# Optimization experiments

Measured on AMD Instinct MI355X. Metric: run time of the kernel, lower is better.

## Reference

```python
import jax, jax.numpy as jnp
import numpy as np

B, SEQ, DIM = 4, 8192, 512
G = 32              # group_size: number of outer chunks (per source rearrange 'b (g n) d')
QK = 128            # query_key_dim
HD = QK // 4        # head_dim = 32 (used for softmax scale)
HEAD_D = 2 * HD     # per-head feature dim = 64 (h=2 heads over QK)
HID = DIM           # expansion_factor = 1.0
EPS = 1e-5


def _shift_seq(t):
    # F.pad(t, (0,0,1,-1)): prepend one zero row along axis=-2, drop last row
    pad = [(0, 0)] * (t.ndim - 2) + [(1, 0), (0, 0)]
    return jnp.pad(t, pad)[..., :-1, :]


def setup_inputs() -> dict:
    key = jax.random.key(0)
    ks = jax.random.split(key, 8)
    s = 0.02
    return {
        "x": jax.random.normal(ks[0], (B, SEQ, DIM), jnp.float32),
        "ln_g": jnp.ones((DIM,), jnp.float32),
        "ln_b": jnp.zeros((DIM,), jnp.float32),
        "w_qk": jax.random.normal(ks[1], (DIM, QK), jnp.float32) * s,
        "g4": jax.random.normal(ks[2], (4, QK), jnp.float32) * s,   # qk_offset_scale.gamma
        "b4": jnp.zeros((4, QK), jnp.float32),                       # qk_offset_scale.beta
        "g2": jax.random.normal(ks[3], (2, QK), jnp.float32) * s,   # shift_one_offset_scale.gamma
        "b2": jnp.zeros((2, QK), jnp.float32),
        "w_hidden": jax.random.normal(ks[4], (DIM, 2 * HID), jnp.float32) * s,
        "w_gate": jax.random.normal(ks[5], (DIM, HID), jnp.float32) * s,
        "w_out": jax.random.normal(ks[6], (5 * HID, DIM), jnp.float32) * s,
    }


def reference(x, ln_g, ln_b, w_qk, g4, b4, g2, b2, w_hidden, w_gate, w_out):
    b, seq, dim = x.shape
    n = seq // G  # tokens per chunk; seq chosen as multiple of G so padding = 0

    # LayerNorm
    mu = jnp.mean(x, axis=-1, keepdims=True)
    var = jnp.var(x, axis=-1, keepdims=True)
    xs = (x - mu) * jax.lax.rsqrt(var + EPS) * ln_g + ln_b

    # token shift of first half of channels (shift_tokens=True)
    half = dim // 2
    xs = jnp.concatenate([_shift_seq(xs[..., :half]), xs[..., half:]], axis=-1)

    qk = xs @ w_qk                                  # [b, seq, QK]
    qk_g = qk.reshape(b, G, n, QK)                  # 'b (g n) d -> b g n d', g outer
    qk_mean = qk_g.mean(axis=2)                     # [b, G, QK]

    # OffsetScale(heads=4) on per-chunk mean -> q_offset, k_offset, q_scale, k_scale
    offs = qk_mean[:, :, None, :] * g4 + b4         # [b, G, 4, QK]
    q_off, k_off, q_sc, k_sc = (offs[:, :, i, :] for i in range(4))

    q = qk_g * q_sc[:, :, None, :] + q_off[:, :, None, :]   # [b, G, n, QK]
    k = qk_g * k_sc[:, :, None, :] + k_off[:, :, None, :]

    # shift-by-one variants within each chunk, re-scaled + shift-one offsets
    q_s_off = qk_mean * g2[0] + b2[0]               # [b, G, QK]
    k_s_off = qk_mean * g2[1] + b2[1]
    qs = _shift_seq(q) * q_sc[:, :, None, :] + q_s_off[:, :, None, :]
    ks_ = _shift_seq(k) * k_sc[:, :, None, :] + k_s_off[:, :, None, :]

    def heads(t):  # [b,G,n,QK] -> [b,G,2,n,HEAD_D]
        return t.reshape(b, G, n, 2, HEAD_D).transpose(0, 1, 3, 2, 4)

    q_all = jnp.concatenate([heads(q), heads(qs)], axis=2)   # [b,G,4,n,64]
    k_all = jnp.concatenate([heads(k), heads(ks_)], axis=2)

    hg = xs @ w_hidden                              # [b, seq, 2*HID]
    hidden, gate = hg[..., :HID], hg[..., HID:]
    hidden_g = hidden.reshape(b, G, n, HID)

    sim = jnp.einsum('bghid,bghjd->bghij', q_all, k_all) * (HD ** -0.5)
    neg = -jnp.finfo(sim.dtype).max
    causal = jnp.triu(jnp.ones((n, n), dtype=bool), 1)  # applied unconditionally in source
    sim = jnp.where(causal, neg, sim)
    attn = jax.nn.softmax(sim, axis=-1)             # dropout=0 (eval)

    out = jnp.einsum('bghij,bgje->bghie', attn, hidden_g)   # [b,G,4,n,HID]
    gate_g = gate.reshape(b, G, n, HID)
    out = jax.nn.silu(out) * gate_g[:, :, None, :, :]
    out = out.transpose(0, 1, 3, 2, 4).reshape(b, seq, 4 * HID)  # 'b g h n e -> b (g n) (h e)'

    residual = jnp.concatenate([hidden, out], axis=-1)       # [b, seq, 5*HID]
    out = residual @ w_out                                   # [b, seq, dim]
    out = out * jax.nn.silu(xs @ w_gate)
    return out + xs
```

## Files before the change

kernel.cpp:

```cpp
#include <hip/hip_runtime.h>
#include <hip/hip_bf16.h>
#include <math.h>

#define BB 4
#define SEQ 8192
#define DIM 512
#define GG 32
#define NPG 256
#define QKD 128
#define HIDD 512

typedef unsigned short u16;
typedef unsigned int u32;

using s16x8 = __attribute__((ext_vector_type(8))) short;
using f32x4 = __attribute__((ext_vector_type(4))) float;

__device__ __forceinline__ float bf2f(u16 u) { return __uint_as_float(((u32)u) << 16); }
__device__ __forceinline__ u16 f2bf(float f) {
  u32 b = __float_as_uint(f);
  return (u16)((b + 0x7FFFu + ((b >> 16) & 1u)) >> 16);
}
__device__ __forceinline__ float silu_f(float x) { return x / (1.f + expf(-x)); }
__device__ __forceinline__ float silu_fast(float x) { return x / (1.f + __expf(-x)); }
__device__ __forceinline__ float4 fma4(float4 a, float4 b, float4 c) {
  return make_float4(a.x*b.x+c.x, a.y*b.y+c.y, a.z*b.z+c.z, a.w*b.w+c.w);
}
__device__ __forceinline__ float4 mul4(float4 a, float4 b) {
  return make_float4(a.x*b.x, a.y*b.y, a.z*b.z, a.w*b.w);
}
#define LD4(p, off) (*(const float4*)((p) + (off)))

__device__ __forceinline__ void gl_lds16(const u16* g, u16* l) {
  __builtin_amdgcn_global_load_lds((const __attribute__((address_space(1))) void*)g,
                                   (__attribute__((address_space(3))) void*)l, 16, 0, 0);
}

__device__ __forceinline__ s16x8 aff8(s16x8 v, float4 s0, float4 s1, float4 o0, float4 o1) {
  union U { s16x8 x; u16 u[8]; };
  U in; in.x = v; U r;
  r.u[0] = f2bf(bf2f(in.u[0]) * s0.x + o0.x);
  r.u[1] = f2bf(bf2f(in.u[1]) * s0.y + o0.y);
  r.u[2] = f2bf(bf2f(in.u[2]) * s0.z + o0.z);
  r.u[3] = f2bf(bf2f(in.u[3]) * s0.w + o0.w);
  r.u[4] = f2bf(bf2f(in.u[4]) * s1.x + o1.x);
  r.u[5] = f2bf(bf2f(in.u[5]) * s1.y + o1.y);
  r.u[6] = f2bf(bf2f(in.u[6]) * s1.z + o1.z);
  r.u[7] = f2bf(bf2f(in.u[7]) * s1.w + o1.w);
  return r.x;
}
__device__ __forceinline__ s16x8 pack8(float4 a, float4 b) {
  union { s16x8 v; u16 u[8]; } z;
  z.u[0] = f2bf(a.x); z.u[1] = f2bf(a.y); z.u[2] = f2bf(a.z); z.u[3] = f2bf(a.w);
  z.u[4] = f2bf(b.x); z.u[5] = f2bf(b.y); z.u[6] = f2bf(b.z); z.u[7] = f2bf(b.w);
  return z.v;
}

__global__ __launch_bounds__(256) void k_ln(const float* __restrict__ x,
    const float* __restrict__ lg, const float* __restrict__ lb,
    float* __restrict__ xs, u16* __restrict__ xsb) {
  const int row = blockIdx.x;
  const int s = row & (SEQ - 1);
  const int t = threadIdx.x;
  const float* xr = x + (size_t)row * DIM;
  float v0 = xr[t], v1 = xr[t + 256];
  float sum = v0 + v1, sq = v0 * v0 + v1 * v1;
  #pragma unroll
  for (int o = 32; o; o >>= 1) { sum += __shfl_down(sum, o); sq += __shfl_down(sq, o); }
  __shared__ float sm[8];
  const int w = t >> 6;
  if ((t & 63) == 0) { sm[w] = sum; sm[4 + w] = sq; }
  __syncthreads();
  if (t == 0) {
    float S = sm[0] + sm[1] + sm[2] + sm[3];
    float Q = sm[4] + sm[5] + sm[6] + sm[7];
    float mu = S * (1.f / DIM);
    float var = Q * (1.f / DIM) - mu * mu;
    sm[0] = mu; sm[4] = rsqrtf(var + 1e-5f);
  }
  __syncthreads();
  const float mu = sm[0], rs = sm[4];
  float y0 = (v0 - mu) * rs * lg[t] + lb[t];
  float y1 = (v1 - mu) * rs * lg[t + 256] + lb[t + 256];
  xs[(size_t)row * DIM + t + 256] = y1;
  xsb[(size_t)row * DIM + t + 256] = f2bf(y1);
  if (s + 1 < SEQ) {
    xs[(size_t)(row + 1) * DIM + t] = y0;
    xsb[(size_t)(row + 1) * DIM + t] = f2bf(y0);
  }
  if (s == 0) { xs[(size_t)row * DIM + t] = 0.f; xsb[(size_t)row * DIM + t] = 0; }
}

__global__ __launch_bounds__(256) void k_trw(const float* __restrict__ src, u16* __restrict__ dst,
    int N, int dstLD, int rowOff) {
  __shared__ u16 T[64][66];
  const int t = threadIdx.x;
  const int k0 = blockIdx.x * 64, n0 = blockIdx.y * 64;
  #pragma unroll
  for (int i = 0; i < 16; ++i) {
    int idx = t + 256 * i;
    int r = idx >> 6, c = idx & 63;
    T[c][r] = f2bf(src[(size_t)(k0 + r) * N + n0 + c]);
  }
  __syncthreads();
  #pragma unroll
  for (int i = 0; i < 16; ++i) {
    int idx = t + 256 * i;
    int r = idx >> 6, c = idx & 63;
    dst[(size_t)(rowOff + n0 + r) * dstLD + k0 + c] = T[r][c];
  }
}

__global__ __launch_bounds__(256) void k_trh(const u16* __restrict__ hidt, u16* __restrict__ hidr) {
  __shared__ u16 T[64][66];
  const int t = threadIdx.x;
  const int j0 = blockIdx.x * 64;
  const int e0 = blockIdx.y * 64;
  const int bg = blockIdx.z;
  #pragma unroll
  for (int i = 0; i < 16; ++i) {
    int idx = t + 256 * i; int r = idx >> 6, c = idx & 63;
    T[c][r] = hidt[((size_t)bg * 512 + e0 + r) * 256 + j0 + c];
  }
  __syncthreads();
  #pragma unroll
  for (int i = 0; i < 16; ++i) {
    int idx = t + 256 * i; int r = idx >> 6, c = idx & 63;
    hidr[((size_t)bg * 256 + j0 + r) * 512 + e0 + c] = T[r][c];
  }
}

__global__ __launch_bounds__(256, 3) void k_gemm1m(const u16* __restrict__ xsb,
    const u16* __restrict__ w1t, u16* __restrict__ qk, u16* __restrict__ hidt,
    u16* __restrict__ gate, u16* __restrict__ xg) {
  __shared__ u16 As[128 * 64];
  __shared__ u16 Bs[128 * 64];
  const int t = threadIdx.x;
  const int blk = blockIdx.x;
  const int xcd = blk & 7;
  const int loc = blk >> 3;
  const int m0 = (xcd * 32 + loc / 13) * 128;
  const int n0 = (loc % 13) * 128;
  const int w = t >> 6, l = t & 63, lr = l & 15, lq = l >> 4;
  const int wr = (w >> 1) * 64, wc = (w & 1) * 64;
  const int rI = l >> 3;
  const int c8 = (l & 7) ^ rI;
  const int slotA = lq ^ (lr & 7);
  const int slotB = (4 + lq) ^ (lr & 7);
  f32x4 acc[4][4];
  #pragma unroll
  for (int i = 0; i < 4; ++i)
    #pragma unroll
    for (int j = 0; j < 4; ++j) acc[i][j] = (f32x4){0.f, 0.f, 0.f, 0.f};
  for (int tt = 0; tt < 8; ++tt) {
    const int k0 = tt * 64;
    #pragma unroll
    for (int i = 0; i < 4; ++i) {
      const int br = w * 32 + i * 8;
      gl_lds16(xsb + (size_t)(m0 + br + rI) * 512 + k0 + c8 * 8, &As[br * 64]);
      gl_lds16(w1t + (size_t)(n0 + br + rI) * 512 + k0 + c8 * 8, &Bs[br * 64]);
    }
    __syncthreads();
    #pragma unroll
    for (int kk = 0; kk < 2; ++kk) {
      const int slot = kk ? slotB : slotA;
      s16x8 af[4], bf[4];
      #pragma unroll
      for (int fi = 0; fi < 4; ++fi) af[fi] = *(const s16x8*)&As[(wr + fi * 16 + lr) * 64 + slot * 8];
      #pragma unroll
      for (int fj = 0; fj < 4; ++fj) bf[fj] = *(const s16x8*)&Bs[(wc + fj * 16 + lr) * 64 + slot * 8];
      #pragma unroll
      for (int fi = 0; fi < 4; ++fi)
        #pragma unroll
        for (int fj = 0; fj < 4; ++fj)
          acc[fi][fj] = __builtin_amdgcn_mfma_f32_16x16x32_bf16(af[fi], bf[fj], acc[fi][fj], 0, 0, 0);
    }
    __syncthreads();
  }
  if (n0 == 0) {
    #pragma unroll
    for (int fi = 0; fi < 4; ++fi)
      #pragma unroll
      for (int fj = 0; fj < 4; ++fj) {
        const int n = wc + fj * 16 + lr;
        const int mb = m0 + wr + fi * 16 + lq * 4;
        #pragma unroll
        for (int r = 0; r < 4; ++r)
          qk[(size_t)(mb + r) * QKD + n] = f2bf(acc[fi][fj][r]);
      }
  } else if (n0 < 640) {
    const int bg = m0 >> 8;
    #pragma unroll
    for (int fi = 0; fi < 4; ++fi)
      #pragma unroll
      for (int fj = 0; fj < 4; ++fj) {
        const int e = n0 - 128 + wc + fj * 16 + lr;
        const int j0 = (m0 & 255) + wr + fi * 16 + lq * 4;
        ushort4 pk;
        pk.x = f2bf(acc[fi][fj][0]); pk.y = f2bf(acc[fi][fj][1]);
        pk.z = f2bf(acc[fi][fj][2]); pk.w = f2bf(acc[fi][fj][3]);
        *(ushort4*)(hidt + ((size_t)bg * 512 + e) * 256 + j0) = pk;
      }
  } else if (n0 < 1152) {
    #pragma unroll
    for (int fi = 0; fi < 4; ++fi)
      #pragma unroll
      for (int fj = 0; fj < 4; ++fj) {
        const int n = n0 - 640 + wc + fj * 16 + lr;
        const int mb = m0 + wr + fi * 16 + lq * 4;
        #pragma unroll
        for (int r = 0; r < 4; ++r)
          gate[(size_t)(mb + r) * HIDD + n] = f2bf(acc[fi][fj][r]);
      }
  } else {
    #pragma unroll
    for (int fi = 0; fi < 4; ++fi)
      #pragma unroll
      for (int fj = 0; fj < 4; ++fj) {
        const int n = n0 - 1152 + wc + fj * 16 + lr;
        const int mb = m0 + wr + fi * 16 + lq * 4;
        #pragma unroll
        for (int r = 0; r < 4; ++r)
          xg[(size_t)(mb + r) * HIDD + n] = f2bf(silu_f(acc[fi][fj][r]));
      }
  }
}

__global__ __launch_bounds__(128) void k_qkmean(const u16* __restrict__ qk, float* __restrict__ qm) {
  const int bg = blockIdx.x;
  const int c = threadIdx.x;
  const u16* p = qk + (size_t)bg * NPG * QKD + c;
  float s = 0.f;
  for (int i = 0; i < NPG; ++i) s += bf2f(p[(size_t)i * QKD]);
  qm[(size_t)bg * QKD + c] = s * (1.f / NPG);
}

__global__ __launch_bounds__(256, 4) void k_attn(const u16* __restrict__ qk,
    const float* __restrict__ qm, const float* __restrict__ g4, const float* __restrict__ b4,
    const float* __restrict__ g2, const float* __restrict__ b2,
    const u16* __restrict__ hidt, const u16* __restrict__ gate, u16* __restrict__ out4) {
  __shared__ u16 Vs[64][264];
  const int t = threadIdx.x;
  const int l = t & 63;
  const int h = t >> 6;
  const bool sh = (h >= 2);
  const int blk = blockIdx.x;
  const int xcd = blk & 7;
  const int bb = blk >> 3;
  const int bg = xcd * 16 + (bb >> 4);
  const int iw = 15 - (bb & 15);
  const size_t grpRow = (size_t)bg * NPG;
  const int cbase = (h & 1) << 6;
  const int lr = l & 15, lq = l >> 4;
  const int cA = cbase + 8 * lq;
  const int ntmax = iw, jtmax = iw >> 1;
  const int irow = iw * 16 + lr;
  const float* qmp = qm + bg * QKD;
  float4 qmA = LD4(qmp, cA),      qmB = LD4(qmp, cA + 4);
  float4 qmC = LD4(qmp, cA + 32), qmD = LD4(qmp, cA + 36);
  float4 qscA = fma4(qmA, LD4(g4, 2*QKD+cA),    LD4(b4, 2*QKD+cA));
  float4 qscB = fma4(qmB, LD4(g4, 2*QKD+cA+4),  LD4(b4, 2*QKD+cA+4));
  float4 qscC = fma4(qmC, LD4(g4, 2*QKD+cA+32), LD4(b4, 2*QKD+cA+32));
  float4 qscD = fma4(qmD, LD4(g4, 2*QKD+cA+36), LD4(b4, 2*QKD+cA+36));
  float4 qofA = fma4(qmA, LD4(g4, cA),      LD4(b4, cA));
  float4 qofB = fma4(qmB, LD4(g4, cA+4),    LD4(b4, cA+4));
  float4 qofC = fma4(qmC, LD4(g4, cA+32),   LD4(b4, cA+32));
  float4 qofD = fma4(qmD, LD4(g4, cA+36),   LD4(b4, cA+36));
  float4 kscA = fma4(qmA, LD4(g4, 3*QKD+cA),    LD4(b4, 3*QKD+cA));
  float4 kscB = fma4(qmB, LD4(g4, 3*QKD+cA+4),  LD4(b4, 3*QKD+cA+4));
  float4 kscC = fma4(qmC, LD4(g4, 3*QKD+cA+32), LD4(b4, 3*QKD+cA+32));
  float4 kscD = fma4(qmD, LD4(g4, 3*QKD+cA+36), LD4(b4, 3*QKD+cA+36));
  float4 kofA = fma4(qmA, LD4(g4, QKD+cA),      LD4(b4, QKD+cA));
  float4 kofB = fma4(qmB, LD4(g4, QKD+cA+4),    LD4(b4, QKD+cA+4));
  float4 kofC = fma4(qmC, LD4(g4, QKD+cA+32),   LD4(b4, QKD+cA+32));
  float4 kofD = fma4(qmD, LD4(g4, QKD+cA+36),   LD4(b4, QKD+cA+36));
  s16x8 qz0 = {0,0,0,0,0,0,0,0}, qz1 = qz0, kz0 = qz0, kz1 = qz0;
  if (sh) {
    float4 qsoA = fma4(qmA, LD4(g2, cA),    LD4(b2, cA));
    float4 qsoB = fma4(qmB, LD4(g2, cA+4),  LD4(b2, cA+4));
    float4 qsoC = fma4(qmC, LD4(g2, cA+32), LD4(b2, cA+32));
    float4 qsoD = fma4(qmD, LD4(g2, cA+36), LD4(b2, cA+36));
    float4 ksoA = fma4(qmA, LD4(g2, QKD+cA),    LD4(b2, QKD+cA));
    float4 ksoB = fma4(qmB, LD4(g2, QKD+cA+4),  LD4(b2, QKD+cA+4));
    float4 ksoC = fma4(qmC, LD4(g2, QKD+cA+32), LD4(b2, QKD+cA+32));
    float4 ksoD = fma4(qmD, LD4(g2, QKD+cA+36), LD4(b2, QKD+cA+36));
    qofA = fma4(qofA, qscA, qsoA); qofB = fma4(qofB, qscB, qsoB);
    qofC = fma4(qofC, qscC, qsoC); qofD = fma4(qofD, qscD, qsoD);
    qscA = mul4(qscA, qscA); qscB = mul4(qscB, qscB);
    qscC = mul4(qscC, qscC); qscD = mul4(qscD, qscD);
    kofA = fma4(kofA, kscA, ksoA); kofB = fma4(kofB, kscB, ksoB);
    kofC = fma4(kofC, kscC, ksoC); kofD = fma4(kofD, kscD, ksoD);
    kscA = mul4(kscA, kscA); kscB = mul4(kscB, kscB);
    kscC = mul4(kscC, kscC); kscD = mul4(kscD, kscD);
    qz0 = pack8(qsoA, qsoB); qz1 = pack8(qsoC, qsoD);
    kz0 = pack8(ksoA, ksoB); kz1 = pack8(ksoC, ksoD);
  }
  const float scl = 0.17677669529663687f;
  const int qsrc = sh ? (irow ? irow - 1 : 0) : irow;
  const u16* qrow = qk + (grpRow + qsrc) * QKD + cA;
  s16x8 qb0 = aff8(*(const s16x8*)qrow,        qscA, qscB, qofA, qofB);
  s16x8 qb1 = aff8(*(const s16x8*)(qrow + 32), qscC, qscD, qofC, qofD);
  if (sh && irow == 0) { qb0 = qz0; qb1 = qz1; }
  f32x4 sfr[16];
  #pragma unroll
  for (int nt = 0; nt < 16; ++nt) if (nt <= ntmax) {
    const int jr = nt * 16 + lr;
    const int ksrc = sh ? (jr ? jr - 1 : 0) : jr;
    const u16* kr = qk + (grpRow + ksrc) * QKD + cA;
    s16x8 ka0 = aff8(*(const s16x8*)kr,        kscA, kscB, kofA, kofB);
    s16x8 ka1 = aff8(*(const s16x8*)(kr + 32), kscC, kscD, kofC, kofD);
    if (sh && jr == 0) { ka0 = kz0; ka1 = kz1; }
    f32x4 c = {0.f, 0.f, 0.f, 0.f};
    c = __builtin_amdgcn_mfma_f32_16x16x32_bf16(ka0, qb0, c, 0, 0, 0);
    c = __builtin_amdgcn_mfma_f32_16x16x32_bf16(ka1, qb1, c, 0, 0, 0);
    sfr[nt] = c;
  }
  float mx = -3.4e38f;
  #pragma unroll
  for (int nt = 0; nt < 16; ++nt) if (nt <= ntmax) {
    #pragma unroll
    for (int r = 0; r < 4; ++r) {
      int j = nt * 16 + lq * 4 + r;
      if (j <= irow) mx = fmaxf(mx, sfr[nt][r] * scl);
    }
  }
  mx = fmaxf(mx, __shfl_xor(mx, 16));
  mx = fmaxf(mx, __shfl_xor(mx, 32));
  float sum = 0.f;
  u32 p01[16], p23[16];
  #pragma unroll
  for (int nt = 0; nt < 16; ++nt) { p01[nt] = 0u; p23[nt] = 0u; }
  #pragma unroll
  for (int nt = 0; nt < 16; ++nt) if (nt <= ntmax) {
    int j = nt * 16 + lq * 4;
    float e0 = (j + 0 <= irow) ? __expf(sfr[nt][0] * scl - mx) : 0.f;
    float e1 = (j + 1 <= irow) ? __expf(sfr[nt][1] * scl - mx) : 0.f;
    float e2 = (j + 2 <= irow) ? __expf(sfr[nt][2] * scl - mx) : 0.f;
    float e3 = (j + 3 <= irow) ? __expf(sfr[nt][3] * scl - mx) : 0.f;
    sum += (e0 + e1) + (e2 + e3);
    p01[nt] = (u32)f2bf(e0) | ((u32)f2bf(e1) << 16);
    p23[nt] = (u32)f2bf(e2) | ((u32)f2bf(e3) << 16);
  }
  sum += __shfl_xor(sum, 16);
  sum += __shfl_xor(sum, 32);
  const float inv = 1.f / sum;
  const int srcA = (l & 15) | ((l & 16) << 1);
  const int srcB = srcA + 16;
  const bool hi = (l >= 32);
  s16x8 bfr[8];
  #pragma unroll
  for (int jt = 0; jt < 8; ++jt) if (jt <= jtmax) {
    u32 a0 = __shfl((int)p01[2 * jt], srcA), a1 = __shfl((int)p23[2 * jt], srcA);
    u32 a2 = __shfl((int)p01[2 * jt], srcB), a3 = __shfl((int)p23[2 * jt], srcB);
    u32 b0 = __shfl((int)p01[2 * jt + 1], srcA), b1 = __shfl((int)p23[2 * jt + 1], srcA);
    u32 b2 = __shfl((int)p01[2 * jt + 1], srcB), b3 = __shfl((int)p23[2 * jt + 1], srcB);
    union { u32 u[4]; s16x8 v; } bb2;
    bb2.u[0] = hi ? b0 : a0; bb2.u[1] = hi ? b1 : a1;
    bb2.u[2] = hi ? b2 : a2; bb2.u[3] = hi ? b3 : a3;
    bfr[jt] = bb2.v;
  }
  const u16* vtb = hidt + (size_t)bg * (512 * 256);
  const size_t srow = grpRow + irow;
  const u16* gp = gate + srow * HIDD;
  u16* op = out4 + srow * 2048 + ((size_t)h << 9);
  for (int oct = 0; oct < 8; ++oct) {
    __syncthreads();
    const u16* src = vtb + (size_t)oct * 64 * 256;
    #pragma unroll
    for (int it = 0; it < 8; ++it) {
      int flat = it * 256 + t;
      int row = flat >> 5, col8 = (flat & 31) * 8;
      *(uint4*)&Vs[row][col8] = *(const uint4*)(src + (size_t)row * 256 + col8);
    }
    __syncthreads();
    f32x4 acc[4];
    #pragma unroll
    for (int ef = 0; ef < 4; ++ef) acc[ef] = (f32x4){0.f, 0.f, 0.f, 0.f};
    #pragma unroll
    for (int jt = 0; jt < 8; ++jt) if (jt <= jtmax) {
      __builtin_amdgcn_s_setprio(1);
      #pragma unroll
      for (int ef = 0; ef < 4; ++ef) {
        s16x8 va = *(const s16x8*)&Vs[ef * 16 + lr][jt * 32 + 8 * lq];
        acc[ef] = __builtin_amdgcn_mfma_f32_16x16x32_bf16(va, bfr[jt], acc[ef], 0, 0, 0);
      }
      __builtin_amdgcn_s_setprio(0);
    }
    #pragma unroll
    for (int ef = 0; ef < 4; ++ef) {
      const int e = oct * 64 + ef * 16 + lq * 4;
      ushort4 gu = *(const ushort4*)(gp + e);
      ushort4 ov;
      ov.x = f2bf(silu_fast(acc[ef][0] * inv) * bf2f(gu.x));
      ov.y = f2bf(silu_fast(acc[ef][1] * inv) * bf2f(gu.y));
      ov.z = f2bf(silu_fast(acc[ef][2] * inv) * bf2f(gu.z));
      ov.w = f2bf(silu_fast(acc[ef][3] * inv) * bf2f(gu.w));
      *(ushort4*)(op + e) = ov;
    }
  }
}

__global__ __launch_bounds__(256, 3) void k_gemm2m(const u16* __restrict__ hidr,
    const u16* __restrict__ out4, const u16* __restrict__ wt,
    const u16* __restrict__ xg, float* __restrict__ out) {
  __shared__ u16 As[128 * 64];
  __shared__ u16 Bs[128 * 64];
  const int t = threadIdx.x;
  const int blk = blockIdx.x;
  const int xcd = blk & 7;
  const int loc = blk >> 3;
  const int m0 = (xcd * 32 + (loc >> 2)) * 128;
  const int n0 = (loc & 3) * 128;
  const int w = t >> 6, l = t & 63, lr = l & 15, lq = l >> 4;
  const int wr = (w >> 1) * 64, wc = (w & 1) * 64;
  const int rI = l >> 3;
  const int c8 = (l & 7) ^ rI;
  const int slotA = lq ^ (lr & 7);
  const int slotB = (4 + lq) ^ (lr & 7);
  f32x4 acc[4][4];
  #pragma unroll
  for (int i = 0; i < 4; ++i)
    #pragma unroll
    for (int j = 0; j < 4; ++j) acc[i][j] = (f32x4){0.f, 0.f, 0.f, 0.f};
  for (int tt = 0; tt < 40; ++tt) {
    const int k0 = tt * 64;
    const u16* ab; size_t ald; int ko;
    if (k0 < 512) { ab = hidr; ald = 512;  ko = k0; }
    else          { ab = out4; ald = 2048; ko = k0 - 512; }
    #pragma unroll
    for (int i = 0; i < 4; ++i) {
      const int br = w * 32 + i * 8;
      gl_lds16(ab + (size_t)(m0 + br + rI) * ald + ko + c8 * 8, &As[br * 64]);
      gl_lds16(wt + (size_t)(n0 + br + rI) * 2560 + k0 + c8 * 8, &Bs[br * 64]);
    }
    __syncthreads();
    #pragma unroll
    for (int kk = 0; kk < 2; ++kk) {
      const int slot = kk ? slotB : slotA;
      s16x8 af[4], bf[4];
      #pragma unroll
      for (int fi = 0; fi < 4; ++fi) af[fi] = *(const s16x8*)&As[(wr + fi * 16 + lr) * 64 + slot * 8];
      #pragma unroll
      for (int fj = 0; fj < 4; ++fj) bf[fj] = *(const s16x8*)&Bs[(wc + fj * 16 + lr) * 64 + slot * 8];
      #pragma unroll
      for (int fi = 0; fi < 4; ++fi)
        #pragma unroll
        for (int fj = 0; fj < 4; ++fj)
          acc[fi][fj] = __builtin_amdgcn_mfma_f32_16x16x32_bf16(af[fi], bf[fj], acc[fi][fj], 0, 0, 0);
    }
    __syncthreads();
  }
  #pragma unroll
  for (int fi = 0; fi < 4; ++fi)
    #pragma unroll
    for (int fj = 0; fj < 4; ++fj) {
      const int n = n0 + wc + fj * 16 + lr;
      const int mb = m0 + wr + fi * 16 + lq * 4;
      #pragma unroll
      for (int r = 0; r < 4; ++r) {
        const size_t idx = (size_t)(mb + r) * DIM + n;
        out[idx] = acc[fi][fj][r] * bf2f(xg[idx]) + out[idx];
      }
    }
}

extern "C" void kernel_launch(void* const* d_in, const int* in_sizes, int n_in,
                              void* d_out, int out_size, void* d_ws, size_t ws_size,
                              hipStream_t stream) {
  const float* x        = (const float*)d_in[0];
  const float* lg       = (const float*)d_in[1];
  const float* lb       = (const float*)d_in[2];
  const float* w_qk     = (const float*)d_in[3];
  const float* g4       = (const float*)d_in[4];
  const float* b4       = (const float*)d_in[5];
  const float* g2       = (const float*)d_in[6];
  const float* b2       = (const float*)d_in[7];
  const float* w_hidden = (const float*)d_in[8];
  const float* w_gate   = (const float*)d_in[9];
  const float* w_out    = (const float*)d_in[10];
  if (ws_size < 247660544ull) return;
  char* ws = (char*)d_ws;
  float* QM   = (float*)(ws + 0);
  u16*   HIDT = (u16*)  (ws + 65536);
  u16*   GATE = (u16*)  (ws + 33619968);
  u16*   XG   = (u16*)  (ws + 67174400);
  u16*   QKb  = (u16*)  (ws + 100728832);
  u16*   W1T  = (u16*)  (ws + 109117440);
  u16*   WT   = (u16*)  (ws + 110821376);
  u16*   OUT4 = (u16*)  (ws + 113442816);
  u16*   XSB  = (u16*)  (ws + 113442816);
  u16*   HIDR = (u16*)  (ws + 33619968);
  float* XS   = (float*)d_out;
  float* OUT  = (float*)d_out;

  k_ln<<<BB * SEQ, 256, 0, stream>>>(x, lg, lb, XS, XSB);
  k_trw<<<dim3(8, 2),  256, 0, stream>>>(w_qk,     W1T, 128,  512,  0);
  k_trw<<<dim3(8, 16), 256, 0, stream>>>(w_hidden, W1T, 1024, 512,  128);
  k_trw<<<dim3(8, 8),  256, 0, stream>>>(w_gate,   W1T, 512,  512,  1152);
  k_trw<<<dim3(40, 8), 256, 0, stream>>>(w_out,    WT,  512,  2560, 0);
  k_gemm1m<<<3328, 256, 0, stream>>>(XSB, W1T, QKb, HIDT, GATE, XG);
  k_qkmean<<<BB * GG, 128, 0, stream>>>(QKb, QM);
  k_attn<<<BB * GG * 16, 256, 0, stream>>>(QKb, QM, g4, b4, g2, b2, HIDT, GATE, OUT4);
  k_trh<<<dim3(4, 8, 128), 256, 0, stream>>>(HIDT, HIDR);
  k_gemm2m<<<1024, 256, 0, stream>>>(HIDR, OUT4, WT, XG, OUT);
}
```

Measured before the change: 403.0 us.

## Fold offset-scale into per-key bias and skip loading unused V columns

```diff
diff --git a/kernel.cpp b/kernel.cpp
--- a/kernel.cpp
+++ b/kernel.cpp
@@ -36,24 +36,18 @@
                                    (__attribute__((address_space(3))) void*)l, 16, 0, 0);
 }
 
-__device__ __forceinline__ s16x8 aff8(s16x8 v, float4 s0, float4 s1, float4 o0, float4 o1) {
+__device__ __forceinline__ s16x8 mul8(s16x8 v, float4 s0, float4 s1) {
   union U { s16x8 x; u16 u[8]; };
   U in; in.x = v; U r;
-  r.u[0] = f2bf(bf2f(in.u[0]) * s0.x + o0.x);
-  r.u[1] = f2bf(bf2f(in.u[1]) * s0.y + o0.y);
-  r.u[2] = f2bf(bf2f(in.u[2]) * s0.z + o0.z);
-  r.u[3] = f2bf(bf2f(in.u[3]) * s0.w + o0.w);
-  r.u[4] = f2bf(bf2f(in.u[4]) * s1.x + o1.x);
-  r.u[5] = f2bf(bf2f(in.u[5]) * s1.y + o1.y);
-  r.u[6] = f2bf(bf2f(in.u[6]) * s1.z + o1.z);
-  r.u[7] = f2bf(bf2f(in.u[7]) * s1.w + o1.w);
+  r.u[0] = f2bf(bf2f(in.u[0]) * s0.x);
+  r.u[1] = f2bf(bf2f(in.u[1]) * s0.y);
+  r.u[2] = f2bf(bf2f(in.u[2]) * s0.z);
+  r.u[3] = f2bf(bf2f(in.u[3]) * s0.w);
+  r.u[4] = f2bf(bf2f(in.u[4]) * s1.x);
+  r.u[5] = f2bf(bf2f(in.u[5]) * s1.y);
+  r.u[6] = f2bf(bf2f(in.u[6]) * s1.z);
+  r.u[7] = f2bf(bf2f(in.u[7]) * s1.w);
   return r.x;
-}
-__device__ __forceinline__ s16x8 pack8(float4 a, float4 b) {
-  union { s16x8 v; u16 u[8]; } z;
-  z.u[0] = f2bf(a.x); z.u[1] = f2bf(a.y); z.u[2] = f2bf(a.z); z.u[3] = f2bf(a.w);
-  z.u[4] = f2bf(b.x); z.u[5] = f2bf(b.y); z.u[6] = f2bf(b.z); z.u[7] = f2bf(b.w);
-  return z.v;
 }
 
 __global__ __launch_bounds__(256) void k_ln(const float* __restrict__ x,
@@ -235,10 +229,50 @@
   qm[(size_t)bg * QKD + c] = s * (1.f / NPG);
 }
 
+__global__ __launch_bounds__(256) void k_bprep(const u16* __restrict__ qk,
+    const float* __restrict__ qm, const float* __restrict__ g4, const float* __restrict__ b4,
+    const float* __restrict__ g2, const float* __restrict__ b2, float* __restrict__ bjs) {
+  const int bg = blockIdx.x;
+  const int t = threadIdx.x;
+  const int h = t >> 6, l = t & 63;
+  const bool sh = (h >= 2);
+  const int cbase = (h & 1) << 6;
+  const size_t grpRow = (size_t)bg * NPG;
+  const int dd = (l & 7) * 8;
+  float c[8];
+  #pragma unroll
+  for (int e = 0; e < 8; ++e) {
+    int d = cbase + dd + e;
+    float qmv = qm[bg * QKD + d];
+    float qsc = qmv * g4[2 * QKD + d] + b4[2 * QKD + d];
+    float qof = qmv * g4[d] + b4[d];
+    float ksc = qmv * g4[3 * QKD + d] + b4[3 * QKD + d];
+    float Oq, Sk;
+    if (!sh) { Oq = qof; Sk = ksc; }
+    else {
+      float qso = qmv * g2[d] + b2[d];
+      Oq = qof * qsc + qso;
+      Sk = ksc * ksc;
+    }
+    c[e] = Oq * Sk;
+  }
+  float* bp = bjs + ((size_t)bg * 4 + h) * NPG;
+  for (int jb = 0; jb < NPG; jb += 8) {
+    int j = jb + (l >> 3);
+    int src = sh ? (j ? j - 1 : 0) : j;
+    const u16* row = qk + (grpRow + src) * QKD + cbase + dd;
+    float s = 0.f;
+    #pragma unroll
+    for (int e = 0; e < 8; ++e) s += bf2f(row[e]) * c[e];
+    s += __shfl_xor(s, 1); s += __shfl_xor(s, 2); s += __shfl_xor(s, 4);
+    if ((l & 7) == 0) bp[j] = s;
+  }
+}
+
 __global__ __launch_bounds__(256, 4) void k_attn(const u16* __restrict__ qk,
     const float* __restrict__ qm, const float* __restrict__ g4, const float* __restrict__ b4,
-    const float* __restrict__ g2, const float* __restrict__ b2,
-    const u16* __restrict__ hidt, const u16* __restrict__ gate, u16* __restrict__ out4) {
+    const float* __restrict__ bjs, const u16* __restrict__ hidt,
+    const u16* __restrict__ gate, u16* __restrict__ out4) {
   __shared__ u16 Vs[64][264];
   const int t = threadIdx.x;
   const int l = t & 63;
@@ -258,61 +292,39 @@
   const float* qmp = qm + bg * QKD;
   float4 qmA = LD4(qmp, cA),      qmB = LD4(qmp, cA + 4);
   float4 qmC = LD4(qmp, cA + 32), qmD = LD4(qmp, cA + 36);
-  float4 qscA = fma4(qmA, LD4(g4, 2*QKD+cA),    LD4(b4, 2*QKD+cA));
-  float4 qscB = fma4(qmB, LD4(g4, 2*QKD+cA+4),  LD4(b4, 2*QKD+cA+4));
-  float4 qscC = fma4(qmC, LD4(g4, 2*QKD+cA+32), LD4(b4, 2*QKD+cA+32));
-  float4 qscD = fma4(qmD, LD4(g4, 2*QKD+cA+36), LD4(b4, 2*QKD+cA+36));
-  float4 qofA = fma4(qmA, LD4(g4, cA),      LD4(b4, cA));
-  float4 qofB = fma4(qmB, LD4(g4, cA+4),    LD4(b4, cA+4));
-  float4 qofC = fma4(qmC, LD4(g4, cA+32),   LD4(b4, cA+32));
-  float4 qofD = fma4(qmD, LD4(g4, cA+36),   LD4(b4, cA+36));
-  float4 kscA = fma4(qmA, LD4(g4, 3*QKD+cA),    LD4(b4, 3*QKD+cA));
-  float4 kscB = fma4(qmB, LD4(g4, 3*QKD+cA+4),  LD4(b4, 3*QKD+cA+4));
-  float4 kscC = fma4(qmC, LD4(g4, 3*QKD+cA+32), LD4(b4, 3*QKD+cA+32));
-  float4 kscD = fma4(qmD, LD4(g4, 3*QKD+cA+36), LD4(b4, 3*QKD+cA+36));
-  float4 kofA = fma4(qmA, LD4(g4, QKD+cA),      LD4(b4, QKD+cA));
-  float4 kofB = fma4(qmB, LD4(g4, QKD+cA+4),    LD4(b4, QKD+cA+4));
-  float4 kofC = fma4(qmC, LD4(g4, QKD+cA+32),   LD4(b4, QKD+cA+32));
-  float4 kofD = fma4(qmD, LD4(g4, QKD+cA+36),   LD4(b4, QKD+cA+36));
-  s16x8 qz0 = {0,0,0,0,0,0,0,0}, qz1 = qz0, kz0 = qz0, kz1 = qz0;
-  if (sh) {
-    float4 qsoA = fma4(qmA, LD4(g2, cA),    LD4(b2, cA));
-    float4 qsoB = fma4(qmB, LD4(g2, cA+4),  LD4(b2, cA+4));
-    float4 qsoC = fma4(qmC, LD4(g2, cA+32), LD4(b2, cA+32));
-    float4 qsoD = fma4(qmD, LD4(g2, cA+36), LD4(b2, cA+36));
-    float4 ksoA = fma4(qmA, LD4(g2, QKD+cA),    LD4(b2, QKD+cA));
-    float4 ksoB = fma4(qmB, LD4(g2, QKD+cA+4),  LD4(b2, QKD+cA+4));
-    float4 ksoC = fma4(qmC, LD4(g2, QKD+cA+32), LD4(b2, QKD+cA+32));
-    float4 ksoD = fma4(qmD, LD4(g2, QKD+cA+36), LD4(b2, QKD+cA+36));
-    qofA = fma4(qofA, qscA, qsoA); qofB = fma4(qofB, qscB, qsoB);
-    qofC = fma4(qofC, qscC, qsoC); qofD = fma4(qofD, qscD, qsoD);
-    qscA = mul4(qscA, qscA); qscB = mul4(qscB, qscB);
-    qscC = mul4(qscC, qscC); qscD = mul4(qscD, qscD);
-    kofA = fma4(kofA, kscA, ksoA); kofB = fma4(kofB, kscB, ksoB);
-    kofC = fma4(kofC, kscC, ksoC); kofD = fma4(kofD, kscD, ksoD);
-    kscA = mul4(kscA, kscA); kscB = mul4(kscB, kscB);
-    kscC = mul4(kscC, kscC); kscD = mul4(kscD, kscD);
-    qz0 = pack8(qsoA, qsoB); qz1 = pack8(qsoC, qsoD);
-    kz0 = pack8(ksoA, ksoB); kz1 = pack8(ksoC, ksoD);
-  }
+  float4 wA = mul4(fma4(qmA, LD4(g4, 2*QKD+cA),    LD4(b4, 2*QKD+cA)),
+                   fma4(qmA, LD4(g4, 3*QKD+cA),    LD4(b4, 3*QKD+cA)));
+  float4 wB = mul4(fma4(qmB, LD4(g4, 2*QKD+cA+4),  LD4(b4, 2*QKD+cA+4)),
+                   fma4(qmB, LD4(g4, 3*QKD+cA+4),  LD4(b4, 3*QKD+cA+4)));
+  float4 wC = mul4(fma4(qmC, LD4(g4, 2*QKD+cA+32), LD4(b4, 2*QKD+cA+32)),
+                   fma4(qmC, LD4(g4, 3*QKD+cA+32), LD4(b4, 3*QKD+cA+32)));
+  float4 wD = mul4(fma4(qmD, LD4(g4, 2*QKD+cA+36), LD4(b4, 2*QKD+cA+36)),
+                   fma4(qmD, LD4(g4, 3*QKD+cA+36), LD4(b4, 3*QKD+cA+36)));
+  if (sh) { wA = mul4(wA, wA); wB = mul4(wB, wB); wC = mul4(wC, wC); wD = mul4(wD, wD); }
   const float scl = 0.17677669529663687f;
   const int qsrc = sh ? (irow ? irow - 1 : 0) : irow;
   const u16* qrow = qk + (grpRow + qsrc) * QKD + cA;
-  s16x8 qb0 = aff8(*(const s16x8*)qrow,        qscA, qscB, qofA, qofB);
-  s16x8 qb1 = aff8(*(const s16x8*)(qrow + 32), qscC, qscD, qofC, qofD);
-  if (sh && irow == 0) { qb0 = qz0; qb1 = qz1; }
+  s16x8 qb0 = mul8(*(const s16x8*)qrow,        wA, wB);
+  s16x8 qb1 = mul8(*(const s16x8*)(qrow + 32), wC, wD);
   f32x4 sfr[16];
   #pragma unroll
   for (int nt = 0; nt < 16; ++nt) if (nt <= ntmax) {
     const int jr = nt * 16 + lr;
     const int ksrc = sh ? (jr ? jr - 1 : 0) : jr;
     const u16* kr = qk + (grpRow + ksrc) * QKD + cA;
-    s16x8 ka0 = aff8(*(const s16x8*)kr,        kscA, kscB, kofA, kofB);
-    s16x8 ka1 = aff8(*(const s16x8*)(kr + 32), kscC, kscD, kofC, kofD);
-    if (sh && jr == 0) { ka0 = kz0; ka1 = kz1; }
+    s16x8 ka0 = *(const s16x8*)kr;
+    s16x8 ka1 = *(const s16x8*)(kr + 32);
     f32x4 c = {0.f, 0.f, 0.f, 0.f};
     c = __builtin_amdgcn_mfma_f32_16x16x32_bf16(ka0, qb0, c, 0, 0, 0);
     c = __builtin_amdgcn_mfma_f32_16x16x32_bf16(ka1, qb1, c, 0, 0, 0);
+    sfr[nt] = c;
+  }
+  const float* bp = bjs + ((size_t)bg * 4 + h) * NPG;
+  #pragma unroll
+  for (int nt = 0; nt < 16; ++nt) if (nt <= ntmax) {
+    float4 bv = LD4(bp, nt * 16 + lq * 4);
+    f32x4 c = sfr[nt];
+    c[0] += bv.x; c[1] += bv.y; c[2] += bv.z; c[3] += bv.w;
     sfr[nt] = c;
   }
   float mx = -3.4e38f;
@@ -363,14 +375,13 @@
   const size_t srow = grpRow + irow;
   const u16* gp = gate + srow * HIDD;
   u16* op = out4 + srow * 2048 + ((size_t)h << 9);
+  const int vrow = t >> 2, vcol8 = (t & 3) * 8;
   for (int oct = 0; oct < 8; ++oct) {
     __syncthreads();
     const u16* src = vtb + (size_t)oct * 64 * 256;
-    #pragma unroll
-    for (int it = 0; it < 8; ++it) {
-      int flat = it * 256 + t;
-      int row = flat >> 5, col8 = (flat & 31) * 8;
-      *(uint4*)&Vs[row][col8] = *(const uint4*)(src + (size_t)row * 256 + col8);
+    for (int jt2 = 0; jt2 <= jtmax; ++jt2) {
+      *(uint4*)&Vs[vrow][jt2 * 32 + vcol8] =
+        *(const uint4*)(src + (size_t)vrow * 256 + jt2 * 32 + vcol8);
     }
     __syncthreads();
     f32x4 acc[4];
@@ -478,7 +489,7 @@
   const float* w_hidden = (const float*)d_in[8];
   const float* w_gate   = (const float*)d_in[9];
   const float* w_out    = (const float*)d_in[10];
-  if (ws_size < 247660544ull) return;
+  if (ws_size < 248184832ull) return;
   char* ws = (char*)d_ws;
   float* QM   = (float*)(ws + 0);
   u16*   HIDT = (u16*)  (ws + 65536);
@@ -490,6 +501,7 @@
   u16*   OUT4 = (u16*)  (ws + 113442816);
   u16*   XSB  = (u16*)  (ws + 113442816);
   u16*   HIDR = (u16*)  (ws + 33619968);
+  float* BJS  = (float*)(ws + 247660544);
   float* XS   = (float*)d_out;
   float* OUT  = (float*)d_out;
 
@@ -500,7 +512,8 @@
   k_trw<<<dim3(40, 8), 256, 0, stream>>>(w_out,    WT,  512,  2560, 0);
   k_gemm1m<<<3328, 256, 0, stream>>>(XSB, W1T, QKb, HIDT, GATE, XG);
   k_qkmean<<<BB * GG, 128, 0, stream>>>(QKb, QM);
-  k_attn<<<BB * GG * 16, 256, 0, stream>>>(QKb, QM, g4, b4, g2, b2, HIDT, GATE, OUT4);
+  k_bprep<<<BB * GG, 256, 0, stream>>>(QKb, QM, g4, b4, g2, b2, BJS);
+  k_attn<<<BB * GG * 16, 256, 0, stream>>>(QKb, QM, g4, b4, BJS, HIDT, GATE, OUT4);
   k_trh<<<dim3(4, 8, 128), 256, 0, stream>>>(HIDT, HIDR);
   k_gemm2m<<<1024, 256, 0, stream>>>(HIDR, OUT4, WT, XG, OUT);
 }
```

After: 403.9 us. Within noise of the previous version (+0.2%).
